# Optimization experiments

Hardware: AMD Instinct MI355X
Metric: run time of the kernel (lower is better)

Reference implementation:

```python
import jax, jax.numpy as jnp
import numpy as np

PAGE_SIZE = 64


def setup_inputs() -> dict:
    key = jax.random.key(0)
    k1, k2, k3 = jax.random.split(key, 3)
    num_slots, max_ctx = 512, 32768
    batch = 256
    req_to_token = jax.random.randint(k1, (num_slots, max_ctx), 0, 2097152, dtype=jnp.int32)
    req_pool_indices = jax.random.randint(k2, (batch,), 0, num_slots, dtype=jnp.int64)
    page_kernel_lens = jax.random.randint(k3, (batch,), 0, max_ctx, dtype=jnp.int64)
    kv_start_idx = jnp.zeros((batch,), dtype=jnp.int32)
    return {
        "req_to_token": req_to_token,
        "req_pool_indices": req_pool_indices,
        "page_kernel_lens": page_kernel_lens,
        "kv_start_idx": kv_start_idx,
    }


def reference(req_to_token, req_pool_indices, page_kernel_lens, kv_start_idx):
    # Static upper bound on number of pages per request.
    max_ctx = req_to_token.shape[1]
    max_num_pages = max_ctx // PAGE_SIZE  # 512

    kv_start = kv_start_idx.astype(jnp.int32)                     # [B]
    lens = page_kernel_lens.astype(jnp.int32)                     # [B]
    num_paged = (lens + PAGE_SIZE - 1) // PAGE_SIZE               # [B]

    # Offset of the first token of each page within the request's row.
    page_ids = jnp.arange(max_num_pages, dtype=jnp.int32)         # [P]
    offs = kv_start[:, None] + page_ids[None, :] * PAGE_SIZE      # [B, P]
    offs = jnp.clip(offs, 0, max_ctx - 1)

    rows = req_to_token[req_pool_indices]                         # [B, max_ctx] gather rows
    data = jnp.take_along_axis(rows, offs, axis=1)                # [B, P]

    valid = page_ids[None, :] < num_paged[:, None]                # [B, P]
    kv_indices = jnp.where(valid, data // PAGE_SIZE, 0).astype(jnp.int64)
    return kv_indices
```

## Files before the change

### kernel.cpp

```cpp
#include <hip/hip_runtime.h>
#include <hip/hip_bf16.h>


#define PAGE_SHIFT 6
#define PAGE_SIZE 64

__global__ void kv_indices_kernel(const int* __restrict__ req_to_token,
                                  const int* __restrict__ req_pool_indices,
                                  const int* __restrict__ page_kernel_lens,
                                  const int* __restrict__ kv_start_idx,
                                  int* __restrict__ out,
                                  int max_ctx, int max_num_pages, int total) {
    int idx = blockIdx.x * blockDim.x + threadIdx.x;
    if (idx >= total) return;
    int b = idx / max_num_pages;
    int p = idx - b * max_num_pages;

    int kv_start  = kv_start_idx[b];
    int len       = page_kernel_lens[b];
    int num_paged = (len + PAGE_SIZE - 1) >> PAGE_SHIFT;

    int off = kv_start + (p << PAGE_SHIFT);
    off = min(max(off, 0), max_ctx - 1);

    int row = req_pool_indices[b];
    int data = req_to_token[(long long)row * (long long)max_ctx + off];

    out[idx] = (p < num_paged) ? (data >> PAGE_SHIFT) : 0;
}

extern "C" void kernel_launch(void* const* d_in, const int* in_sizes, int n_in,
                              void* d_out, int out_size, void* d_ws, size_t ws_size,
                              hipStream_t stream) {
    const int* req_to_token     = (const int*)d_in[0];
    const int* req_pool_indices = (const int*)d_in[1];
    const int* page_kernel_lens = (const int*)d_in[2];
    const int* kv_start_idx     = (const int*)d_in[3];
    int*       out              = (int*)d_out;

    int batch         = in_sizes[1];
    int max_num_pages = out_size / batch;
    int max_ctx       = max_num_pages * PAGE_SIZE;
    int total         = out_size;

    int block = 256;
    int grid  = (total + block - 1) / block;
    kv_indices_kernel<<<grid, block, 0, stream>>>(
        req_to_token, req_pool_indices, page_kernel_lens, kv_start_idx,
        out, max_ctx, max_num_pages, total);
}
```

Measured before the change: 91.00 us.

## Map one block per request, skip invalid-page gathers, and vectorize stores

Launches one block per batch entry with each thread producing four consecutive pages. Gathers from req_to_token happen only for pages below the request's page count, so unused pages are no longer loaded. Per-request values are loaded once per thread and results are written as int4. It assumes the page count is a multiple of four and fits in one block.

```diff
diff --git a/kernel.cpp b/kernel.cpp
--- a/kernel.cpp
+++ b/kernel.cpp
@@ -3,30 +3,37 @@
 
 
 #define PAGE_SHIFT 6
-#define PAGE_SIZE 64
+#define PAGE_SIZE  64
 
 __global__ void kv_indices_kernel(const int* __restrict__ req_to_token,
                                   const int* __restrict__ req_pool_indices,
                                   const int* __restrict__ page_kernel_lens,
                                   const int* __restrict__ kv_start_idx,
                                   int* __restrict__ out,
-                                  int max_ctx, int max_num_pages, int total) {
-    int idx = blockIdx.x * blockDim.x + threadIdx.x;
-    if (idx >= total) return;
-    int b = idx / max_num_pages;
-    int p = idx - b * max_num_pages;
+                                  int max_ctx) {
+    const int b  = blockIdx.x;
+    const int p0 = threadIdx.x << 2;
 
-    int kv_start  = kv_start_idx[b];
-    int len       = page_kernel_lens[b];
-    int num_paged = (len + PAGE_SIZE - 1) >> PAGE_SHIFT;
+    const int kv_start  = kv_start_idx[b];
+    const int len       = page_kernel_lens[b];
+    const int num_paged = (len + 63) >> PAGE_SHIFT;
+    const long long rowbase = (long long)req_pool_indices[b] * (long long)max_ctx;
 
-    int off = kv_start + (p << PAGE_SHIFT);
-    off = min(max(off, 0), max_ctx - 1);
+    int r[4];
+    #pragma unroll
+    for (int j = 0; j < 4; ++j) {
+        const int p = p0 + j;
+        int v = 0;
+        if (p < num_paged) {
+            int off = kv_start + (p << PAGE_SHIFT);
+            off = min(max(off, 0), max_ctx - 1);
+            v = req_to_token[rowbase + off] >> PAGE_SHIFT;
+        }
+        r[j] = v;
+    }
 
-    int row = req_pool_indices[b];
-    int data = req_to_token[(long long)row * (long long)max_ctx + off];
-
-    out[idx] = (p < num_paged) ? (data >> PAGE_SHIFT) : 0;
+    int4 packed = make_int4(r[0], r[1], r[2], r[3]);
+    reinterpret_cast<int4*>(out)[(size_t)b * blockDim.x + threadIdx.x] = packed;
 }
 
 extern "C" void kernel_launch(void* const* d_in, const int* in_sizes, int n_in,
@@ -41,11 +48,10 @@
     int batch         = in_sizes[1];
     int max_num_pages = out_size / batch;
     int max_ctx       = max_num_pages * PAGE_SIZE;
-    int total         = out_size;
+    (void)ws_size; (void)d_ws; (void)n_in;
 
-    int block = 256;
-    int grid  = (total + block - 1) / block;
-    kv_indices_kernel<<<grid, block, 0, stream>>>(
+    int block = max_num_pages / 4;
+    kv_indices_kernel<<<batch, block, 0, stream>>>(
         req_to_token, req_pool_indices, page_kernel_lens, kv_start_idx,
-        out, max_ctx, max_num_pages, total);
+        out, max_ctx);
 }
```

New measurement: 92.60 us. No clear change (+1.8%).
